# Optimization experiments

Measured on AMD Instinct MI355X. Metric: run time of the kernel, lower is better.

## Reference

```python
import jax, jax.numpy as jnp
import numpy as np

N_NODES = 50000
N_EDGES = 800000
IN_CH = 128
HIDDEN = 128
OUT_CH = 2
NUM_GRAPHS = 64


def setup_inputs() -> dict:
    key = jax.random.key(0)
    ks = jax.random.split(key, 12)
    x = jax.random.normal(ks[0], (N_NODES, IN_CH), dtype=jnp.float32)
    edge_index = jax.random.randint(ks[1], (2, N_EDGES), 0, N_NODES, dtype=jnp.int32)
    batch = jnp.sort(jax.random.randint(ks[2], (N_NODES,), 0, NUM_GRAPHS, dtype=jnp.int32))
    def glorot(k, fan_in, fan_out):
        s = (6.0 / (fan_in + fan_out)) ** 0.5
        return jax.random.uniform(k, (fan_in, fan_out), jnp.float32, -s, s)
    return {
        "x": x,
        "edge_index": edge_index,
        "batch": batch,
        "W1": glorot(ks[3], IN_CH, HIDDEN), "b1": jnp.zeros((HIDDEN,), jnp.float32),
        "W2": glorot(ks[4], HIDDEN, HIDDEN), "b2": jnp.zeros((HIDDEN,), jnp.float32),
        "W3": glorot(ks[5], HIDDEN, HIDDEN), "b3": jnp.zeros((HIDDEN,), jnp.float32),
        "Wc": glorot(ks[6], HIDDEN, OUT_CH), "bc": jnp.zeros((OUT_CH,), jnp.float32),
    }


def reference(x, edge_index, batch, W1, b1, W2, b2, W3, b3, Wc, bc):
    N = x.shape[0]
    src, dst = edge_index[0], edge_index[1]
    # GCN symmetric normalization with self-loops (PyG GCNConv default):
    # deg[i] = 1 (self loop) + in-degree
    deg = jax.ops.segment_sum(jnp.ones_like(src, jnp.float32), dst, num_segments=N) + 1.0
    dinv = deg ** -0.5                      # [N]
    edge_norm = (dinv[src] * dinv[dst])[:, None]   # [E,1]
    self_norm = (dinv * dinv)[:, None]             # [N,1]

    def gcn(h, W, b):
        hw = h @ W                                                    # [N,D]
        agg = jax.ops.segment_sum(edge_norm * hw[src], dst, num_segments=N)
        return agg + self_norm * hw + b

    h = jax.nn.relu(gcn(x, W1, b1))
    h = jax.nn.relu(gcn(h, W2, b2))
    h = jax.nn.relu(gcn(h, W3, b3))

    # global_mean_pool over batch ids
    counts = jax.ops.segment_sum(jnp.ones((N,), jnp.float32), batch, num_segments=NUM_GRAPHS)
    pooled = jax.ops.segment_sum(h, batch, num_segments=NUM_GRAPHS)
    pooled = pooled / jnp.maximum(counts, 1.0)[:, None]               # [G,D]

    return pooled @ Wc + bc                                           # [G,out]
```

## Files before the change

kernel.cpp:

```cpp
#include <hip/hip_runtime.h>

#define NCH 128
#define NGRAPH 64
#define SUB 16
#define CAP 64

typedef _Float16 h8 __attribute__((ext_vector_type(8)));
typedef float f32x4 __attribute__((ext_vector_type(4)));
typedef float f32x2 __attribute__((ext_vector_type(2)));


__device__ __forceinline__ unsigned pkh(float a, float b) {
    union { _Float16 h[2]; unsigned u; } x;
    x.h[0] = (_Float16)a; x.h[1] = (_Float16)b;
    return x.u;
}
__device__ __forceinline__ float flo(unsigned u) {
    union { unsigned u; _Float16 h[2]; } x; x.u = u; return (float)x.h[0];
}
__device__ __forceinline__ float fhi(unsigned u) {
    union { unsigned u; _Float16 h[2]; } x; x.u = u; return (float)x.h[1];
}
__device__ __forceinline__ unsigned short h16(float a) {
    union { _Float16 h; unsigned short s; } x; x.h = (_Float16)a; return x.s;
}

__device__ __forceinline__ float dinv_of(int cur, int n) {
    return rsqrtf((float)(cur - n * CAP) + 1.0f);
}


__global__ __launch_bounds__(256) void k_setup(const float* __restrict__ W1,
                                               const float* __restrict__ W2,
                                               const float* __restrict__ W3,
                                               uint4* __restrict__ wfrag,
                                               const int* __restrict__ batch,
                                               int* __restrict__ gstart,
                                               int* __restrict__ cursor, int N, int gN) {
    if (blockIdx.x < 24) {
        int gid = blockIdx.x * 256 + threadIdx.x;
        int layer = gid >> 11;
        int fr = gid & 2047;
        int c = fr >> 9;
        int nt = (fr >> 6) & 7;
        int i = fr & 63;
        int nl = i >> 2, q = i & 3;
        int iS = i ^ ((nl >> 1) & 7);
        int n = nt * 16 + nl;
        int k0 = c * 32 + q * 8;
        const float* W = (layer == 0) ? W1 : (layer == 1) ? W2 : W3;
        union { unsigned short s[8]; uint4 u; } pk;
        #pragma unroll
        for (int j = 0; j < 8; j++)
            pk.s[j] = h16(W[(k0 + j) * NCH + n]);
        wfrag[layer * 2048 + (c * 8 + nt) * 64 + iS] = pk.u;
    } else if (blockIdx.x < 24 + gN) {
        int i = (blockIdx.x - 24) * 256 + threadIdx.x;
        if (i >= N) return;
        int b = batch[i];
        int prev = (i == 0) ? -1 : batch[i - 1];
        for (int g = prev + 1; g <= b; g++) gstart[g] = i;
        if (i == N - 1) {
            for (int g = b + 1; g <= NGRAPH; g++) gstart[g] = N;
        }
    } else {
        int i = (blockIdx.x - 24 - gN) * 256 + threadIdx.x;
        if (i < N) cursor[i] = i * CAP;
    }
}

__global__ __launch_bounds__(256) void k_fill(const int* __restrict__ src,
                                              const int* __restrict__ dst,
                                              int* __restrict__ cursor,
                                              int* __restrict__ edge_src, int E, int N) {
    int range = blockIdx.x & 7;
    int chunk = blockIdx.x >> 3;
    int r0 = (range * N) >> 3;
    int r1 = ((range + 1) * N) >> 3;
    int e = chunk * 256 + threadIdx.x;
    if (e >= E) return;
    int d = dst[e];
    if (d >= r0 && d < r1) {
        int p = atomicAdd(&cursor[d], 1);
        if (p < (d + 1) * CAP) edge_src[p] = src[e];
    }
}


__global__ __launch_bounds__(256) void k_mmgemm(const void* __restrict__ Araw,
                                                const uint4* __restrict__ wfrag,
                                                const int* __restrict__ cursor,
                                                unsigned* __restrict__ D, int N,
                                                int a_fp32) {
    __shared__ uint4 Wl[2048];
    int t = threadIdx.x;
    #pragma unroll
    for (int i = 0; i < 8; i++) Wl[i * 256 + t] = wfrag[i * 256 + t];

    int wv = t >> 6, lane = t & 63;
    int rowW = blockIdx.x * 64 + wv * 16;
    int m = lane & 15, q = lane >> 4;
    int aRow = rowW + m;

    union { uint4 u; h8 h; } a[4];
    if (a_fp32) {
        const float* Af = (const float*)Araw;
        #pragma unroll
        for (int c = 0; c < 4; c++) {
            union { _Float16 h[8]; uint4 u; } pk;
            #pragma unroll
            for (int j = 0; j < 8; j++) pk.h[j] = (_Float16)0.f;
            if (aRow < N) {
                float4 v0 = *reinterpret_cast<const float4*>(&Af[(size_t)aRow * NCH + c * 32 + q * 8]);
                float4 v1 = *reinterpret_cast<const float4*>(&Af[(size_t)aRow * NCH + c * 32 + q * 8 + 4]);
                pk.h[0] = (_Float16)v0.x; pk.h[1] = (_Float16)v0.y;
                pk.h[2] = (_Float16)v0.z; pk.h[3] = (_Float16)v0.w;
                pk.h[4] = (_Float16)v1.x; pk.h[5] = (_Float16)v1.y;
                pk.h[6] = (_Float16)v1.z; pk.h[7] = (_Float16)v1.w;
            }
            a[c].u = pk.u;
        }
    } else {
        const unsigned* A = (const unsigned*)Araw;
        #pragma unroll
        for (int c = 0; c < 4; c++) {
            a[c].u = make_uint4(0, 0, 0, 0);
            if (aRow < N)
                a[c].u = *reinterpret_cast<const uint4*>(&A[(size_t)aRow * 64 + c * 16 + q * 4]);
        }
    }

    __syncthreads();

    int iS = (m * 4 + q) ^ ((m >> 1) & 7);

    f32x4 acc[8];
    #pragma unroll
    for (int nt = 0; nt < 8; nt++) acc[nt] = (f32x4){0.f, 0.f, 0.f, 0.f};

    #pragma unroll
    for (int c = 0; c < 4; c++) {
        #pragma unroll
        for (int nt = 0; nt < 8; nt++) {
            union { uint4 u; h8 h; } b;
            b.u = Wl[(c * 8 + nt) * 64 + iS];
            acc[nt] = __builtin_amdgcn_mfma_f32_16x16x32_f16(a[c].h, b.h, acc[nt], 0, 0, 0);
        }
    }

    float dn[4];
    #pragma unroll
    for (int r = 0; r < 4; r++) {
        int rg = rowW + q * 4 + r;
        dn[r] = (rg < N) ? dinv_of(cursor[rg], rg) : 0.0f;
    }
    #pragma unroll
    for (int nt = 0; nt < 8; nt++) {
        #pragma unroll
        for (int r = 0; r < 4; r++) {
            int rg = rowW + q * 4 + r;
            float v = acc[nt][r] * dn[r];
            unsigned b = __builtin_amdgcn_cvt_pk_fp8_f32(v, v, 0, false) & 0xffu;
            b |= ((unsigned)__shfl_xor((int)b, 1, 64)) << 8;
            b |= ((unsigned)__shfl_xor((int)b, 2, 64)) << 16;
            if ((lane & 3) == 0 && rg <= N)
                D[(size_t)rg * 32 + nt * 4 + (m >> 2)] = b;
        }
    }
}


__global__ __launch_bounds__(256) void k_gather(const unsigned short* __restrict__ hw,
                                                const float* __restrict__ bias,
                                                const int* __restrict__ cursor,
                                                const int* __restrict__ edge_src,
                                                unsigned* __restrict__ out, int N) {
    int wv = threadIdx.x >> 6;
    int lane = threadIdx.x & 63;
    int n = blockIdx.x * 4 + wv;
    if (n >= N) return;

    unsigned vs = hw[(size_t)n * 64 + lane];
    f32x2 v0 = __builtin_amdgcn_cvt_pk_f32_fp8((int)vs, false);
    float ax = v0.x, ay = v0.y;

    int j0 = n * CAP;
    int cur = cursor[n];
    int j1 = cur;
    if (j1 > j0 + CAP) j1 = j0 + CAP;
    int j = j0;
    for (; j + 15 < j1; j += 16) {
        unsigned u[16];
        #pragma unroll
        for (int i = 0; i < 16; i++)
            u[i] = hw[(size_t)edge_src[j + i] * 64 + lane];
        #pragma unroll
        for (int i = 0; i < 16; i++) {
            f32x2 v = __builtin_amdgcn_cvt_pk_f32_fp8((int)u[i], false);
            ax += v.x; ay += v.y;
        }
    }
    for (; j + 7 < j1; j += 8) {
        unsigned u[8];
        #pragma unroll
        for (int i = 0; i < 8; i++)
            u[i] = hw[(size_t)edge_src[j + i] * 64 + lane];
        #pragma unroll
        for (int i = 0; i < 8; i++) {
            f32x2 v = __builtin_amdgcn_cvt_pk_f32_fp8((int)u[i], false);
            ax += v.x; ay += v.y;
        }
    }
    for (; j + 1 < j1; j += 2) {
        unsigned u0 = hw[(size_t)edge_src[j + 0] * 64 + lane];
        unsigned u1 = hw[(size_t)edge_src[j + 1] * 64 + lane];
        f32x2 w0 = __builtin_amdgcn_cvt_pk_f32_fp8((int)u0, false);
        f32x2 w1 = __builtin_amdgcn_cvt_pk_f32_fp8((int)u1, false);
        ax += w0.x + w1.x;
        ay += w0.y + w1.y;
    }
    if (j < j1) {
        unsigned u0 = hw[(size_t)edge_src[j] * 64 + lane];
        f32x2 w0 = __builtin_amdgcn_cvt_pk_f32_fp8((int)u0, false);
        ax += w0.x; ay += w0.y;
    }
    float dn = dinv_of(cur, n);
    float2 bb = reinterpret_cast<const float2*>(bias)[lane];
    float ox = fmaxf(ax * dn + bb.x, 0.0f);
    float oy = fmaxf(ay * dn + bb.y, 0.0f);
    out[(size_t)n * 64 + lane] = pkh(ox, oy);
}


__global__ __launch_bounds__(256) void k_poolA(const unsigned* __restrict__ h,
                                               const int* __restrict__ gstart,
                                               float* __restrict__ partial) {
    int g = blockIdx.x >> 4;
    int s = blockIdx.x & (SUB - 1);
    int c2 = threadIdx.x & 63;
    int r = threadIdx.x >> 6;
    int j0 = gstart[g], j1 = gstart[g + 1];
    int len = j1 - j0;
    int chunk = (len + SUB - 1) / SUB;
    int a0 = j0 + s * chunk;
    int a1 = a0 + chunk; if (a1 > j1) a1 = j1;
    float ax = 0.0f, ay = 0.0f;
    for (int j = a0 + r; j < a1; j += 4) {
        unsigned u = h[(size_t)j * 64 + c2];
        ax += flo(u); ay += fhi(u);
    }
    __shared__ float2 sh[4][64];
    sh[r][c2] = make_float2(ax, ay);
    __syncthreads();
    if (r == 0) {
        float sx = sh[0][c2].x + sh[1][c2].x + sh[2][c2].x + sh[3][c2].x;
        float sy = sh[0][c2].y + sh[1][c2].y + sh[2][c2].y + sh[3][c2].y;
        reinterpret_cast<float2*>(partial)[(size_t)(g * SUB + s) * 64 + c2] =
            make_float2(sx, sy);
    }
}

__global__ __launch_bounds__(128) void k_finalize(const float* __restrict__ partial,
                                                  const int* __restrict__ gstart,
                                                  const float* __restrict__ Wc,
                                                  const float* __restrict__ bc,
                                                  float* __restrict__ out) {
    int g = blockIdx.x;
    int c = threadIdx.x;
    float s = 0.0f;
    #pragma unroll
    for (int i = 0; i < SUB; i++) s += partial[(size_t)(g * SUB + i) * NCH + c];
    int len = gstart[g + 1] - gstart[g];
    __shared__ float sh[128];
    sh[c] = s / fmaxf((float)len, 1.0f);
    __syncthreads();
    if (c < 2) {
        float o = 0.0f;
        for (int k = 0; k < NCH; k++) o += sh[k] * Wc[k * 2 + c];
        out[g * 2 + c] = o + bc[c];
    }
}


extern "C" void kernel_launch(void* const* d_in, const int* in_sizes, int n_in,
                              void* d_out, int out_size, void* d_ws, size_t ws_size,
                              hipStream_t stream) {
    const float* x   = (const float*)d_in[0];
    const int* eidx  = (const int*)d_in[1];
    const int* batch = (const int*)d_in[2];
    const float* W1 = (const float*)d_in[3];
    const float* b1 = (const float*)d_in[4];
    const float* W2 = (const float*)d_in[5];
    const float* b2 = (const float*)d_in[6];
    const float* W3 = (const float*)d_in[7];
    const float* b3 = (const float*)d_in[8];
    const float* Wc = (const float*)d_in[9];
    const float* bc = (const float*)d_in[10];
    float* out = (float*)d_out;

    int N = in_sizes[0] / NCH;
    int E = in_sizes[1] / 2;
    const int* src = eidx;
    const int* dst = eidx + E;

    char* w = (char*)d_ws;
    auto alloc = [&](size_t bytes) -> void* {
        void* p = (void*)w;
        w += (bytes + 511) & ~(size_t)511;
        return p;
    };
    int*      cursor    = (int*)alloc((size_t)N * 4);
    int*      edge_src  = (int*)alloc((size_t)N * CAP * 4);
    uint4*    wfrag     = (uint4*)alloc((size_t)3 * 2048 * 16);
    unsigned* hwD       = (unsigned*)alloc((size_t)(N + 64) * 128);
    unsigned* hbA       = (unsigned*)alloc((size_t)N * 64 * 4);
    unsigned* hbB       = (unsigned*)alloc((size_t)N * 64 * 4);
    float*    partial   = (float*)alloc((size_t)NGRAPH * SUB * NCH * 4);
    int*      gstart    = (int*)alloc((size_t)(NGRAPH + 1) * 4);

    int gE = (E + 255) / 256;
    int gN = (N + 255) / 256;

    k_setup<<<24 + 2 * gN, 256, 0, stream>>>(W1, W2, W3, wfrag, batch, gstart, cursor, N, gN);
    k_fill<<<gE * 8, 256, 0, stream>>>(src, dst, cursor, edge_src, E, N);

    int gM = (N + 63) / 64;
    int gA = (N + 3) / 4;
    k_mmgemm<<<gM, 256, 0, stream>>>(x, wfrag, cursor, hwD, N, 1);
    k_gather<<<gA, 256, 0, stream>>>((const unsigned short*)hwD, b1, cursor, edge_src, hbA, N);
    k_mmgemm<<<gM, 256, 0, stream>>>(hbA, wfrag + 2048, cursor, hwD, N, 0);
    k_gather<<<gA, 256, 0, stream>>>((const unsigned short*)hwD, b2, cursor, edge_src, hbB, N);
    k_mmgemm<<<gM, 256, 0, stream>>>(hbB, wfrag + 4096, cursor, hwD, N, 0);
    k_gather<<<gA, 256, 0, stream>>>((const unsigned short*)hwD, b3, cursor, edge_src, hbA, N);

    k_poolA<<<NGRAPH * SUB, 256, 0, stream>>>(hbA, gstart, partial);
    k_finalize<<<NGRAPH, 128, 0, stream>>>(partial, gstart, Wc, bc, out);
}
```

Baseline: 257.7 us.

## Store hidden activations as fp8 and vectorize edge fill with int4 loads

Gather outputs are now written as packed fp8 pairs instead of fp16 pairs, which halves the intermediate activation traffic. The following GEMM decodes that fp8 back to fp16 for MFMA, and the pooling kernel reads fp8 as well. The edge-fill kernel now handles four edges per thread using int4 dst loads, and several loads and stores gain nontemporal hints. This adds another quantization step on the hidden activations, so accuracy may drop.

```diff
diff --git a/kernel.cpp b/kernel.cpp
--- a/kernel.cpp
+++ b/kernel.cpp
@@ -77,12 +77,23 @@
     int chunk = blockIdx.x >> 3;
     int r0 = (range * N) >> 3;
     int r1 = ((range + 1) * N) >> 3;
-    int e = chunk * 256 + threadIdx.x;
+    int e = (chunk * 256 + threadIdx.x) * 4;
     if (e >= E) return;
-    int d = dst[e];
-    if (d >= r0 && d < r1) {
-        int p = atomicAdd(&cursor[d], 1);
-        if (p < (d + 1) * CAP) edge_src[p] = src[e];
+    int d[4];
+    if (e + 3 < E) {
+        int4 t = *reinterpret_cast<const int4*>(&dst[e]);
+        d[0] = t.x; d[1] = t.y; d[2] = t.z; d[3] = t.w;
+    } else {
+        #pragma unroll
+        for (int i = 0; i < 4; i++) d[i] = (e + i < E) ? dst[e + i] : -1;
+    }
+    #pragma unroll
+    for (int i = 0; i < 4; i++) {
+        int di = d[i];
+        if (di >= r0 && di < r1) {
+            int p = atomicAdd(&cursor[di], 1);
+            if (p < (di + 1) * CAP) edge_src[p] = src[e + i];
+        }
     }
 }
 
@@ -121,12 +132,26 @@
             a[c].u = pk.u;
         }
     } else {
-        const unsigned* A = (const unsigned*)Araw;
+        const unsigned* A8 = (const unsigned*)Araw;
         #pragma unroll
         for (int c = 0; c < 4; c++) {
-            a[c].u = make_uint4(0, 0, 0, 0);
-            if (aRow < N)
-                a[c].u = *reinterpret_cast<const uint4*>(&A[(size_t)aRow * 64 + c * 16 + q * 4]);
+            union { _Float16 h[8]; uint4 u; } pk;
+            #pragma unroll
+            for (int j = 0; j < 8; j++) pk.h[j] = (_Float16)0.f;
+            if (aRow < N) {
+                unsigned long long rv = __builtin_nontemporal_load(
+                    reinterpret_cast<const unsigned long long*>(&A8[(size_t)aRow * 32 + c * 8 + q * 2]));
+                unsigned lo = (unsigned)rv, hi = (unsigned)(rv >> 32);
+                f32x2 p0 = __builtin_amdgcn_cvt_pk_f32_fp8((int)lo, false);
+                f32x2 p1 = __builtin_amdgcn_cvt_pk_f32_fp8((int)lo, true);
+                f32x2 p2 = __builtin_amdgcn_cvt_pk_f32_fp8((int)hi, false);
+                f32x2 p3 = __builtin_amdgcn_cvt_pk_f32_fp8((int)hi, true);
+                pk.h[0] = (_Float16)p0.x; pk.h[1] = (_Float16)p0.y;
+                pk.h[2] = (_Float16)p1.x; pk.h[3] = (_Float16)p1.y;
+                pk.h[4] = (_Float16)p2.x; pk.h[5] = (_Float16)p2.y;
+                pk.h[6] = (_Float16)p3.x; pk.h[7] = (_Float16)p3.y;
+            }
+            a[c].u = pk.u;
         }
     }
 
@@ -163,7 +188,7 @@
             unsigned b = __builtin_amdgcn_cvt_pk_fp8_f32(v, v, 0, false) & 0xffu;
             b |= ((unsigned)__shfl_xor((int)b, 1, 64)) << 8;
             b |= ((unsigned)__shfl_xor((int)b, 2, 64)) << 16;
-            if ((lane & 3) == 0 && rg <= N)
+            if ((lane & 3) == 0 && rg < N)
                 D[(size_t)rg * 32 + nt * 4 + (m >> 2)] = b;
         }
     }
@@ -174,7 +199,7 @@
                                                 const float* __restrict__ bias,
                                                 const int* __restrict__ cursor,
                                                 const int* __restrict__ edge_src,
-                                                unsigned* __restrict__ out, int N) {
+                                                unsigned short* __restrict__ out, int N) {
     int wv = threadIdx.x >> 6;
     int lane = threadIdx.x & 63;
     int n = blockIdx.x * 4 + wv;
@@ -193,7 +218,7 @@
         unsigned u[16];
         #pragma unroll
         for (int i = 0; i < 16; i++)
-            u[i] = hw[(size_t)edge_src[j + i] * 64 + lane];
+            u[i] = hw[(size_t)__builtin_nontemporal_load(&edge_src[j + i]) * 64 + lane];
         #pragma unroll
         for (int i = 0; i < 16; i++) {
             f32x2 v = __builtin_amdgcn_cvt_pk_f32_fp8((int)u[i], false);
@@ -204,7 +229,7 @@
         unsigned u[8];
         #pragma unroll
         for (int i = 0; i < 8; i++)
-            u[i] = hw[(size_t)edge_src[j + i] * 64 + lane];
+            u[i] = hw[(size_t)__builtin_nontemporal_load(&edge_src[j + i]) * 64 + lane];
         #pragma unroll
         for (int i = 0; i < 8; i++) {
             f32x2 v = __builtin_amdgcn_cvt_pk_f32_fp8((int)u[i], false);
@@ -212,15 +237,15 @@
         }
     }
     for (; j + 1 < j1; j += 2) {
-        unsigned u0 = hw[(size_t)edge_src[j + 0] * 64 + lane];
-        unsigned u1 = hw[(size_t)edge_src[j + 1] * 64 + lane];
+        unsigned u0 = hw[(size_t)__builtin_nontemporal_load(&edge_src[j + 0]) * 64 + lane];
+        unsigned u1 = hw[(size_t)__builtin_nontemporal_load(&edge_src[j + 1]) * 64 + lane];
         f32x2 w0 = __builtin_amdgcn_cvt_pk_f32_fp8((int)u0, false);
         f32x2 w1 = __builtin_amdgcn_cvt_pk_f32_fp8((int)u1, false);
         ax += w0.x + w1.x;
         ay += w0.y + w1.y;
     }
     if (j < j1) {
-        unsigned u0 = hw[(size_t)edge_src[j] * 64 + lane];
+        unsigned u0 = hw[(size_t)__builtin_nontemporal_load(&edge_src[j]) * 64 + lane];
         f32x2 w0 = __builtin_amdgcn_cvt_pk_f32_fp8((int)u0, false);
         ax += w0.x; ay += w0.y;
     }
@@ -228,11 +253,12 @@
     float2 bb = reinterpret_cast<const float2*>(bias)[lane];
     float ox = fmaxf(ax * dn + bb.x, 0.0f);
     float oy = fmaxf(ay * dn + bb.y, 0.0f);
-    out[(size_t)n * 64 + lane] = pkh(ox, oy);
-}
-
-
-__global__ __launch_bounds__(256) void k_poolA(const unsigned* __restrict__ h,
+    unsigned short o = (unsigned short)(__builtin_amdgcn_cvt_pk_fp8_f32(ox, oy, 0, false) & 0xffff);
+    __builtin_nontemporal_store(o, &out[(size_t)n * 64 + lane]);
+}
+
+
+__global__ __launch_bounds__(256) void k_poolA(const unsigned short* __restrict__ h,
                                                const int* __restrict__ gstart,
                                                float* __restrict__ partial) {
     int g = blockIdx.x >> 4;
@@ -246,8 +272,9 @@
     int a1 = a0 + chunk; if (a1 > j1) a1 = j1;
     float ax = 0.0f, ay = 0.0f;
     for (int j = a0 + r; j < a1; j += 4) {
-        unsigned u = h[(size_t)j * 64 + c2];
-        ax += flo(u); ay += fhi(u);
+        unsigned u = __builtin_nontemporal_load(&h[(size_t)j * 64 + c2]);
+        f32x2 v = __builtin_amdgcn_cvt_pk_f32_fp8((int)u, false);
+        ax += v.x; ay += v.y;
     }
     __shared__ float2 sh[4][64];
     sh[r][c2] = make_float2(ax, ay);
@@ -309,20 +336,20 @@
         w += (bytes + 511) & ~(size_t)511;
         return p;
     };
-    int*      cursor    = (int*)alloc((size_t)N * 4);
-    int*      edge_src  = (int*)alloc((size_t)N * CAP * 4);
-    uint4*    wfrag     = (uint4*)alloc((size_t)3 * 2048 * 16);
-    unsigned* hwD       = (unsigned*)alloc((size_t)(N + 64) * 128);
-    unsigned* hbA       = (unsigned*)alloc((size_t)N * 64 * 4);
-    unsigned* hbB       = (unsigned*)alloc((size_t)N * 64 * 4);
-    float*    partial   = (float*)alloc((size_t)NGRAPH * SUB * NCH * 4);
-    int*      gstart    = (int*)alloc((size_t)(NGRAPH + 1) * 4);
-
-    int gE = (E + 255) / 256;
+    int*            cursor   = (int*)alloc((size_t)N * 4);
+    int*            edge_src = (int*)alloc((size_t)N * CAP * 4);
+    uint4*          wfrag    = (uint4*)alloc((size_t)3 * 2048 * 16);
+    unsigned*       hwD      = (unsigned*)alloc((size_t)(N + 64) * 128);
+    unsigned short* hbA      = (unsigned short*)alloc((size_t)N * 128);
+    unsigned short* hbB      = (unsigned short*)alloc((size_t)N * 128);
+    float*          partial  = (float*)alloc((size_t)NGRAPH * SUB * NCH * 4);
+    int*            gstart   = (int*)alloc((size_t)(NGRAPH + 1) * 4);
+
+    int gE4 = (E + 1023) / 1024;
     int gN = (N + 255) / 256;
 
     k_setup<<<24 + 2 * gN, 256, 0, stream>>>(W1, W2, W3, wfrag, batch, gstart, cursor, N, gN);
-    k_fill<<<gE * 8, 256, 0, stream>>>(src, dst, cursor, edge_src, E, N);
+    k_fill<<<gE4 * 8, 256, 0, stream>>>(src, dst, cursor, edge_src, E, N);
 
     int gM = (N + 63) / 64;
     int gA = (N + 3) / 4;
```

Result: slower. 275.5 us (+6.9%).

## Split FP8 feature table into two channel halves and gather each separately

Applied to the files above, without the earlier changes.

The GEMM now writes the FP8 transformed features as two separate tables of 64 channels each (64 bytes per row) instead of one 128-byte row. Each layer's gather runs twice, once per half, with each lane handling one channel and writing one fp16 output. The aim is to halve the random-access footprint per gather pass so the table fits better in cache. In exchange it doubles gather launches and edge_src reads, and each lane now issues byte loads that move less data per load.

```diff
diff --git a/kernel.cpp b/kernel.cpp
--- a/kernel.cpp
+++ b/kernel.cpp
@@ -154,8 +154,10 @@
         int rg = rowW + q * 4 + r;
         dn[r] = (rg < N) ? dinv_of(cursor[rg], rg) : 0.0f;
     }
+    size_t tabDw = (size_t)(N + 64) * 16;
     #pragma unroll
     for (int nt = 0; nt < 8; nt++) {
+        unsigned* Dt = D + (nt >> 2) * tabDw;
         #pragma unroll
         for (int r = 0; r < 4; r++) {
             int rg = rowW + q * 4 + r;
@@ -163,26 +165,27 @@
             unsigned b = __builtin_amdgcn_cvt_pk_fp8_f32(v, v, 0, false) & 0xffu;
             b |= ((unsigned)__shfl_xor((int)b, 1, 64)) << 8;
             b |= ((unsigned)__shfl_xor((int)b, 2, 64)) << 16;
-            if ((lane & 3) == 0 && rg <= N)
-                D[(size_t)rg * 32 + nt * 4 + (m >> 2)] = b;
-        }
-    }
-}
-
-
-__global__ __launch_bounds__(256) void k_gather(const unsigned short* __restrict__ hw,
+            if ((lane & 3) == 0 && rg < N)
+                Dt[(size_t)rg * 16 + (nt & 3) * 4 + (m >> 2)] = b;
+        }
+    }
+}
+
+
+__global__ __launch_bounds__(256) void k_gather(const unsigned char* __restrict__ hw,
                                                 const float* __restrict__ bias,
                                                 const int* __restrict__ cursor,
                                                 const int* __restrict__ edge_src,
-                                                unsigned* __restrict__ out, int N) {
+                                                unsigned short* __restrict__ out,
+                                                int N, int half) {
     int wv = threadIdx.x >> 6;
     int lane = threadIdx.x & 63;
     int n = blockIdx.x * 4 + wv;
     if (n >= N) return;
-
-    unsigned vs = hw[(size_t)n * 64 + lane];
-    f32x2 v0 = __builtin_amdgcn_cvt_pk_f32_fp8((int)vs, false);
-    float ax = v0.x, ay = v0.y;
+    const unsigned char* tab = hw + (size_t)half * (size_t)(N + 64) * 64;
+
+    f32x2 v0 = __builtin_amdgcn_cvt_pk_f32_fp8((int)tab[(size_t)n * 64 + lane], false);
+    float ax = v0.x;
 
     int j0 = n * CAP;
     int cur = cursor[n];
@@ -193,42 +196,40 @@
         unsigned u[16];
         #pragma unroll
         for (int i = 0; i < 16; i++)
-            u[i] = hw[(size_t)edge_src[j + i] * 64 + lane];
+            u[i] = tab[(size_t)edge_src[j + i] * 64 + lane];
         #pragma unroll
         for (int i = 0; i < 16; i++) {
             f32x2 v = __builtin_amdgcn_cvt_pk_f32_fp8((int)u[i], false);
-            ax += v.x; ay += v.y;
+            ax += v.x;
         }
     }
     for (; j + 7 < j1; j += 8) {
         unsigned u[8];
         #pragma unroll
         for (int i = 0; i < 8; i++)
-            u[i] = hw[(size_t)edge_src[j + i] * 64 + lane];
+            u[i] = tab[(size_t)edge_src[j + i] * 64 + lane];
         #pragma unroll
         for (int i = 0; i < 8; i++) {
             f32x2 v = __builtin_amdgcn_cvt_pk_f32_fp8((int)u[i], false);
-            ax += v.x; ay += v.y;
+            ax += v.x;
         }
     }
     for (; j + 1 < j1; j += 2) {
-        unsigned u0 = hw[(size_t)edge_src[j + 0] * 64 + lane];
-        unsigned u1 = hw[(size_t)edge_src[j + 1] * 64 + lane];
+        unsigned u0 = tab[(size_t)edge_src[j + 0] * 64 + lane];
+        unsigned u1 = tab[(size_t)edge_src[j + 1] * 64 + lane];
         f32x2 w0 = __builtin_amdgcn_cvt_pk_f32_fp8((int)u0, false);
         f32x2 w1 = __builtin_amdgcn_cvt_pk_f32_fp8((int)u1, false);
         ax += w0.x + w1.x;
-        ay += w0.y + w1.y;
     }
     if (j < j1) {
-        unsigned u0 = hw[(size_t)edge_src[j] * 64 + lane];
+        unsigned u0 = tab[(size_t)edge_src[j] * 64 + lane];
         f32x2 w0 = __builtin_amdgcn_cvt_pk_f32_fp8((int)u0, false);
-        ax += w0.x; ay += w0.y;
+        ax += w0.x;
     }
     float dn = dinv_of(cur, n);
-    float2 bb = reinterpret_cast<const float2*>(bias)[lane];
-    float ox = fmaxf(ax * dn + bb.x, 0.0f);
-    float oy = fmaxf(ay * dn + bb.y, 0.0f);
-    out[(size_t)n * 64 + lane] = pkh(ox, oy);
+    float bb = bias[half * 64 + lane];
+    float ox = fmaxf(ax * dn + bb, 0.0f);
+    out[(size_t)n * 128 + half * 64 + lane] = h16(ox);
 }
 
 
@@ -309,14 +310,14 @@
         w += (bytes + 511) & ~(size_t)511;
         return p;
     };
-    int*      cursor    = (int*)alloc((size_t)N * 4);
-    int*      edge_src  = (int*)alloc((size_t)N * CAP * 4);
-    uint4*    wfrag     = (uint4*)alloc((size_t)3 * 2048 * 16);
-    unsigned* hwD       = (unsigned*)alloc((size_t)(N + 64) * 128);
-    unsigned* hbA       = (unsigned*)alloc((size_t)N * 64 * 4);
-    unsigned* hbB       = (unsigned*)alloc((size_t)N * 64 * 4);
-    float*    partial   = (float*)alloc((size_t)NGRAPH * SUB * NCH * 4);
-    int*      gstart    = (int*)alloc((size_t)(NGRAPH + 1) * 4);
+    int*            cursor   = (int*)alloc((size_t)N * 4);
+    int*            edge_src = (int*)alloc((size_t)N * CAP * 4);
+    uint4*          wfrag    = (uint4*)alloc((size_t)3 * 2048 * 16);
+    unsigned*       hwD      = (unsigned*)alloc((size_t)2 * (N + 64) * 64);
+    unsigned short* hbA      = (unsigned short*)alloc((size_t)N * 256);
+    unsigned short* hbB      = (unsigned short*)alloc((size_t)N * 256);
+    float*          partial  = (float*)alloc((size_t)NGRAPH * SUB * NCH * 4);
+    int*            gstart   = (int*)alloc((size_t)(NGRAPH + 1) * 4);
 
     int gE = (E + 255) / 256;
     int gN = (N + 255) / 256;
@@ -326,13 +327,17 @@
 
     int gM = (N + 63) / 64;
     int gA = (N + 3) / 4;
+    const unsigned char* hw8 = (const unsigned char*)hwD;
     k_mmgemm<<<gM, 256, 0, stream>>>(x, wfrag, cursor, hwD, N, 1);
-    k_gather<<<gA, 256, 0, stream>>>((const unsigned short*)hwD, b1, cursor, edge_src, hbA, N);
+    k_gather<<<gA, 256, 0, stream>>>(hw8, b1, cursor, edge_src, hbA, N, 0);
+    k_gather<<<gA, 256, 0, stream>>>(hw8, b1, cursor, edge_src, hbA, N, 1);
     k_mmgemm<<<gM, 256, 0, stream>>>(hbA, wfrag + 2048, cursor, hwD, N, 0);
-    k_gather<<<gA, 256, 0, stream>>>((const unsigned short*)hwD, b2, cursor, edge_src, hbB, N);
+    k_gather<<<gA, 256, 0, stream>>>(hw8, b2, cursor, edge_src, hbB, N, 0);
+    k_gather<<<gA, 256, 0, stream>>>(hw8, b2, cursor, edge_src, hbB, N, 1);
     k_mmgemm<<<gM, 256, 0, stream>>>(hbB, wfrag + 4096, cursor, hwD, N, 0);
-    k_gather<<<gA, 256, 0, stream>>>((const unsigned short*)hwD, b3, cursor, edge_src, hbA, N);
-
-    k_poolA<<<NGRAPH * SUB, 256, 0, stream>>>(hbA, gstart, partial);
+    k_gather<<<gA, 256, 0, stream>>>(hw8, b3, cursor, edge_src, hbA, N, 0);
+    k_gather<<<gA, 256, 0, stream>>>(hw8, b3, cursor, edge_src, hbA, N, 1);
+
+    k_poolA<<<NGRAPH * SUB, 256, 0, stream>>>((const unsigned*)hbA, gstart, partial);
     k_finalize<<<NGRAPH, 128, 0, stream>>>(partial, gstart, Wc, bc, out);
 }
```

Measured after the change: 316.5 us. +22.8%, slower.
